# Optimization experiments

Hardware: AMD Instinct MI355X
Metric: run time of the kernel (lower is better)

The kernel has to match this reference:

```python
import jax, jax.numpy as jnp
import numpy as np
from jax import lax

NUM_POINTS = 2048  # M, from init_kwargs


def setup_inputs() -> dict:
    key = jax.random.key(0)
    points = jax.random.normal(key, (16, 65536, 3), dtype=jnp.float32)
    return {"points": points}


def farthest_point_sampling(points, num_samples):
    """Iterative D-FPS. points: (B, N, 3) -> indices (B, M) int32."""
    B, N, _ = points.shape
    BIG = jnp.asarray(1e10, points.dtype)

    def step(carry, _):
        min_dist, last_idx = carry          # (B, N), (B,)
        last_pt = jnp.take_along_axis(points, last_idx[:, None, None], axis=1)  # (B,1,3)
        d = jnp.sum((points - last_pt) ** 2, axis=-1)  # (B, N) squared dist to newest centroid
        min_dist = jnp.minimum(min_dist, d)
        nxt = jnp.argmax(min_dist, axis=1).astype(jnp.int32)  # farthest remaining point
        return (min_dist, nxt), nxt

    first = jnp.zeros((B,), dtype=jnp.int32)  # seed with point 0 (standard FPS convention)
    init = (jnp.full((B, N), BIG, points.dtype), first)
    _, rest = lax.scan(step, init, None, length=num_samples - 1)  # (M-1, B)
    indices = jnp.concatenate([first[None, :], rest], axis=0)      # (M, B)
    return indices.T                                                # (B, M)


def reference(points):
    B, N, _ = points.shape
    if N <= NUM_POINTS:
        idx = jnp.broadcast_to(jnp.arange(N, dtype=jnp.int32)[None, :], (B, N))
        return idx
    return farthest_point_sampling(points, NUM_POINTS)
```

## Files before the change

kernel.cpp:

```cpp
#include <hip/hip_runtime.h>


#define N_PTS   65536
#define M_SAMP  2048
#define NT      512
#define BPB     16
#define PTS_BLK (N_PTS / BPB)
#define PPT     (PTS_BLK / NT)
#define NWAVES  (NT / 64)
#define NBATCH  16
#define SLOT_U64 16
#define NWORK   (BPB * NBATCH)
#define NHEAT   256
#define DONE_MAGIC 0x600D600D600D600Dull

typedef unsigned long long u64;

__device__ __forceinline__ u64 ld_agent(const u64* a) {
  return __hip_atomic_load(a, __ATOMIC_RELAXED, __HIP_MEMORY_SCOPE_AGENT);
}
__device__ __forceinline__ void st_agent(u64* a, u64 v) {
  __hip_atomic_store(a, v, __ATOMIC_RELAXED, __HIP_MEMORY_SCOPE_AGENT);
}
__device__ __forceinline__ u64* done_word(u64* ws, int b) {
  return ws + (size_t)b * BPB * SLOT_U64 + 12;
}

__global__ __launch_bounds__(NT, 2)
void fps_multi(const float* __restrict__ pts, int* __restrict__ out,
               u64* __restrict__ ws) {
  const int t = threadIdx.x;

  if (blockIdx.x >= NWORK) {
    __builtin_amdgcn_s_setprio(0);
    float a0 = 1.0f + t, a1 = 2.0f + t, a2 = 3.0f, a3 = 4.0f;
    float a4 = 5.0f, a5 = 6.0f, a6 = 7.0f, a7 = 8.0f;
    const float k0 = 1.0000001f, k1 = 0.9999991f;
    for (;;) {
      for (int it = 0; it < 128; ++it) {
        a0 = __builtin_fmaf(a0, k0, k1); a1 = __builtin_fmaf(a1, k0, k1);
        a2 = __builtin_fmaf(a2, k0, k1); a3 = __builtin_fmaf(a3, k0, k1);
        a4 = __builtin_fmaf(a4, k0, k1); a5 = __builtin_fmaf(a5, k0, k1);
        a6 = __builtin_fmaf(a6, k0, k1); a7 = __builtin_fmaf(a7, k0, k1);
      }
      const u64 w = ld_agent(done_word(ws, t & 15));
      if (__all(w == DONE_MAGIC)) break;
    }
    const float s = ((a0 + a1) + (a2 + a3)) + ((a4 + a5) + (a6 + a7));
    if (s == -1234.56789f) st_agent(done_word(ws, t & 15) + 1, (u64)t);
    return;
  }

  __builtin_amdgcn_s_setprio(3);
  const int rank = blockIdx.x & (BPB - 1);
  const int b    = blockIdx.x >> 4;
  const float* __restrict__ p = pts + (size_t)b * (size_t)(N_PTS * 3);
  int* __restrict__ o = out + (size_t)b * M_SAMP;
  const int base = rank * PTS_BLK;

  __shared__ float s_pts[PTS_BLK * 3];
  __shared__ u64   s_bv[NWAVES];
  __shared__ int   s_bi[NWAVES];
  __shared__ float s_c[3];

  for (int i = t; i < PTS_BLK * 3; i += NT)
    s_pts[i] = p[base * 3 + i];
  if (rank == 0 && t == 0) o[0] = 0;
  if (t == 0) { s_c[0] = p[0]; s_c[1] = p[1]; s_c[2] = p[2]; }
  __syncthreads();

  double pd[PPT][3];
  double md[PPT];
#pragma unroll
  for (int j = 0; j < PPT; ++j) {
    const int l = t + j * NT;
    pd[j][0] = (double)s_pts[3 * l + 0];
    pd[j][1] = (double)s_pts[3 * l + 1];
    pd[j][2] = (double)s_pts[3 * l + 2];
    md[j] = 1e10;
  }

  for (int m = 1; m < M_SAMP; ++m) {
    const double cx = (double)s_c[0];
    const double cy = (double)s_c[1];
    const double cz = (double)s_c[2];

    u64 bestb = 0;
    int besti = base + t;

#pragma unroll
    for (int j = 0; j < PPT; ++j) {
      const double dx = __dsub_rn(pd[j][0], cx);
      const double dy = __dsub_rn(pd[j][1], cy);
      const double dz = __dsub_rn(pd[j][2], cz);
      const double d  = __dadd_rn(__dadd_rn(__dmul_rn(dx, dx),
                                            __dmul_rn(dy, dy)),
                                  __dmul_rn(dz, dz));
      const double nmd = fmin(md[j], d);
      md[j] = nmd;
      const u64 nb = (u64)__double_as_longlong(nmd);
      if (nb > bestb) { bestb = nb; besti = base + t + j * NT; }
    }

#pragma unroll
    for (int off = 32; off >= 1; off >>= 1) {
      const u64 ov = __shfl_xor(bestb, off, 64);
      const int oi = __shfl_xor(besti, off, 64);
      if (ov > bestb || (ov == bestb && oi < besti)) { bestb = ov; besti = oi; }
    }
    if ((t & 63) == 0) { s_bv[t >> 6] = bestb; s_bi[t >> 6] = besti; }
    __syncthreads();

    if (t < 64) {
      if (t < NWAVES) {
        bestb = s_bv[t]; besti = s_bi[t];
#pragma unroll
        for (int off = NWAVES / 2; off >= 1; off >>= 1) {
          const u64 ov = __shfl_xor(bestb, off, 64);
          const int oi = __shfl_xor(besti, off, 64);
          if (ov > bestb || (ov == bestb && oi < besti)) { bestb = ov; besti = oi; }
        }
      }
      const u64 mm  = (u64)(unsigned)m;
      const u64 grp = (u64)(((m & 1) * NBATCH + b) * BPB);
      if (t == 0) {
        u64* slot = ws + (grp + rank) * SLOT_U64;
        const int l = besti - base;
        const unsigned xb = __float_as_uint(s_pts[3 * l + 0]);
        const unsigned yb = __float_as_uint(s_pts[3 * l + 1]);
        const unsigned zb = __float_as_uint(s_pts[3 * l + 2]);
        const u64 ti = (mm << 16) | (u64)(unsigned)besti;
        st_agent(&slot[0], (bestb << 32) | ti);
        st_agent(&slot[1], (bestb & 0xFFFFFFFF00000000ull) | ti);
        st_agent(&slot[2], ((u64)xb << 32) | (mm << 16) | (u64)(yb >> 16));
        st_agent(&slot[3], ((u64)(yb & 0xFFFFu) << 48) | ((u64)zb << 16) | mm);
      }
      if (t < BPB) {
        const u64* rs = ws + (grp + t) * SLOT_U64;
        u64 A, B, C, D;
        for (;;) {
          A = ld_agent(rs + 0);
          B = ld_agent(rs + 1);
          C = ld_agent(rs + 2);
          D = ld_agent(rs + 3);
          const bool ok = (((A >> 16) & 0xFFFFull) == mm) &
                          (((B >> 16) & 0xFFFFull) == mm) &
                          (((C >> 16) & 0xFFFFull) == mm) &
                          ((D & 0xFFFFull) == mm);
          if (ok) break;
        }
        u64 v = (B & 0xFFFFFFFF00000000ull) | (A >> 32);
        int i = (int)(A & 0xFFFFull);
        float fx = __uint_as_float((unsigned)(C >> 32));
        float fy = __uint_as_float((unsigned)(((C & 0xFFFFull) << 16) | (D >> 48)));
        float fz = __uint_as_float((unsigned)((D >> 16) & 0xFFFFFFFFull));
        int r = t;
#pragma unroll
        for (int off = BPB / 2; off >= 1; off >>= 1) {
          const u64 ov = __shfl_xor(v, off, 64);
          const int oi = __shfl_xor(i, off, 64);
          const int orr = __shfl_xor(r, off, 64);
          if (ov > v || (ov == v && oi < i)) { v = ov; i = oi; r = orr; }
        }
        fx = __shfl(fx, r, 64);
        fy = __shfl(fy, r, 64);
        fz = __shfl(fz, r, 64);
        if (t == 0) {
          s_c[0] = fx; s_c[1] = fy; s_c[2] = fz;
          if (rank == 0) o[m] = i;
        }
      }
    }
    __syncthreads();
  }

  if (rank == 0 && t == 0) st_agent(done_word(ws, b), DONE_MAGIC);
}

extern "C" void kernel_launch(void* const* d_in, const int* in_sizes, int n_in,
                              void* d_out, int out_size, void* d_ws, size_t ws_size,
                              hipStream_t stream) {
  const float* pts = (const float*)d_in[0];
  int* out = (int*)d_out;
  hipLaunchKernelGGL(fps_multi, dim3(NWORK + NHEAT), dim3(NT), 0, stream,
                     pts, out, (u64*)d_ws);
}
```

Baseline: 6.138 ms.

## Remove heater blocks and drop per-iteration second barrier via redundant per-wave exchange

Every wave now redundantly performs the block-level reduction and polls the cross-block workspace slots itself. The centroid is then broadcast within each wave through shuffles instead of shared memory. This removes the second __syncthreads per sample iteration, with per-wave partial results double-buffered by iteration parity to avoid races. It also deletes the extra spinning 'heater' blocks and their done-flag signalling. The trade-off is that many more waves poll global memory concurrently, and any clock or priority effect the heater blocks had is lost.

```diff
diff --git a/kernel.cpp b/kernel.cpp
--- a/kernel.cpp
+++ b/kernel.cpp
@@ -10,9 +10,6 @@
 #define NWAVES  (NT / 64)
 #define NBATCH  16
 #define SLOT_U64 16
-#define NWORK   (BPB * NBATCH)
-#define NHEAT   256
-#define DONE_MAGIC 0x600D600D600D600Dull
 
 typedef unsigned long long u64;
 
@@ -22,51 +19,27 @@
 __device__ __forceinline__ void st_agent(u64* a, u64 v) {
   __hip_atomic_store(a, v, __ATOMIC_RELAXED, __HIP_MEMORY_SCOPE_AGENT);
 }
-__device__ __forceinline__ u64* done_word(u64* ws, int b) {
-  return ws + (size_t)b * BPB * SLOT_U64 + 12;
-}
 
 __global__ __launch_bounds__(NT, 2)
 void fps_multi(const float* __restrict__ pts, int* __restrict__ out,
                u64* __restrict__ ws) {
-  const int t = threadIdx.x;
-
-  if (blockIdx.x >= NWORK) {
-    __builtin_amdgcn_s_setprio(0);
-    float a0 = 1.0f + t, a1 = 2.0f + t, a2 = 3.0f, a3 = 4.0f;
-    float a4 = 5.0f, a5 = 6.0f, a6 = 7.0f, a7 = 8.0f;
-    const float k0 = 1.0000001f, k1 = 0.9999991f;
-    for (;;) {
-      for (int it = 0; it < 128; ++it) {
-        a0 = __builtin_fmaf(a0, k0, k1); a1 = __builtin_fmaf(a1, k0, k1);
-        a2 = __builtin_fmaf(a2, k0, k1); a3 = __builtin_fmaf(a3, k0, k1);
-        a4 = __builtin_fmaf(a4, k0, k1); a5 = __builtin_fmaf(a5, k0, k1);
-        a6 = __builtin_fmaf(a6, k0, k1); a7 = __builtin_fmaf(a7, k0, k1);
-      }
-      const u64 w = ld_agent(done_word(ws, t & 15));
-      if (__all(w == DONE_MAGIC)) break;
-    }
-    const float s = ((a0 + a1) + (a2 + a3)) + ((a4 + a5) + (a6 + a7));
-    if (s == -1234.56789f) st_agent(done_word(ws, t & 15) + 1, (u64)t);
-    return;
-  }
-
-  __builtin_amdgcn_s_setprio(3);
   const int rank = blockIdx.x & (BPB - 1);
   const int b    = blockIdx.x >> 4;
   const float* __restrict__ p = pts + (size_t)b * (size_t)(N_PTS * 3);
   int* __restrict__ o = out + (size_t)b * M_SAMP;
+  const int t    = threadIdx.x;
+  const int lane = t & 63;
+  const int wave = t >> 6;
   const int base = rank * PTS_BLK;
 
   __shared__ float s_pts[PTS_BLK * 3];
-  __shared__ u64   s_bv[NWAVES];
-  __shared__ int   s_bi[NWAVES];
-  __shared__ float s_c[3];
+  __shared__ u64   s_wv[2][NWAVES];
+  __shared__ int   s_wi[2][NWAVES];
 
   for (int i = t; i < PTS_BLK * 3; i += NT)
     s_pts[i] = p[base * 3 + i];
   if (rank == 0 && t == 0) o[0] = 0;
-  if (t == 0) { s_c[0] = p[0]; s_c[1] = p[1]; s_c[2] = p[2]; }
+  float c0 = p[0], c1 = p[1], c2 = p[2];
   __syncthreads();
 
   double pd[PPT][3];
@@ -81,9 +54,9 @@
   }
 
   for (int m = 1; m < M_SAMP; ++m) {
-    const double cx = (double)s_c[0];
-    const double cy = (double)s_c[1];
-    const double cz = (double)s_c[2];
+    const double cx = (double)c0;
+    const double cy = (double)c1;
+    const double cz = (double)c2;
 
     u64 bestb = 0;
     int besti = base + t;
@@ -108,73 +81,76 @@
       const int oi = __shfl_xor(besti, off, 64);
       if (ov > bestb || (ov == bestb && oi < besti)) { bestb = ov; besti = oi; }
     }
-    if ((t & 63) == 0) { s_bv[t >> 6] = bestb; s_bi[t >> 6] = besti; }
+
+    const int par = m & 1;
+    if (lane == 0) { s_wv[par][wave] = bestb; s_wi[par][wave] = besti; }
     __syncthreads();
 
-    if (t < 64) {
-      if (t < NWAVES) {
-        bestb = s_bv[t]; besti = s_bi[t];
+    u64 bb; int bi;
+    if (lane < NWAVES) { bb = s_wv[par][lane]; bi = s_wi[par][lane]; }
+    else               { bb = 0;               bi = 0x7FFFFFFF; }
 #pragma unroll
-        for (int off = NWAVES / 2; off >= 1; off >>= 1) {
-          const u64 ov = __shfl_xor(bestb, off, 64);
-          const int oi = __shfl_xor(besti, off, 64);
-          if (ov > bestb || (ov == bestb && oi < besti)) { bestb = ov; besti = oi; }
-        }
+    for (int off = NWAVES / 2; off >= 1; off >>= 1) {
+      const u64 ov = __shfl_xor(bb, off, 64);
+      const int oi = __shfl_xor(bi, off, 64);
+      if (ov > bb || (ov == bb && oi < bi)) { bb = ov; bi = oi; }
+    }
+
+    const u64 mm  = (u64)(unsigned)m;
+    const u64 grp = (u64)((par * NBATCH + b) * BPB);
+    if (t == 0) {
+      u64* slot = ws + (grp + rank) * SLOT_U64;
+      const int l = bi - base;
+      const unsigned xb = __float_as_uint(s_pts[3 * l + 0]);
+      const unsigned yb = __float_as_uint(s_pts[3 * l + 1]);
+      const unsigned zb = __float_as_uint(s_pts[3 * l + 2]);
+      const u64 ti = (mm << 16) | (u64)(unsigned)bi;
+      st_agent(&slot[0], (bb << 32) | ti);
+      st_agent(&slot[1], (bb & 0xFFFFFFFF00000000ull) | ti);
+      st_agent(&slot[2], ((u64)xb << 32) | (mm << 16) | (u64)(yb >> 16));
+      st_agent(&slot[3], ((u64)(yb & 0xFFFFu) << 48) | ((u64)zb << 16) | mm);
+    }
+
+    float fx = 0.0f, fy = 0.0f, fz = 0.0f;
+    int   wi = 0;
+    if (lane < BPB) {
+      const u64* rs = ws + (grp + lane) * SLOT_U64;
+      u64 A, B, C, D;
+      for (;;) {
+        A = ld_agent(rs + 0);
+        B = ld_agent(rs + 1);
+        C = ld_agent(rs + 2);
+        D = ld_agent(rs + 3);
+        const bool ok = (((A >> 16) & 0xFFFFull) == mm) &
+                        (((B >> 16) & 0xFFFFull) == mm) &
+                        (((C >> 16) & 0xFFFFull) == mm) &
+                        ((D & 0xFFFFull) == mm);
+        if (ok) break;
       }
-      const u64 mm  = (u64)(unsigned)m;
-      const u64 grp = (u64)(((m & 1) * NBATCH + b) * BPB);
-      if (t == 0) {
-        u64* slot = ws + (grp + rank) * SLOT_U64;
-        const int l = besti - base;
-        const unsigned xb = __float_as_uint(s_pts[3 * l + 0]);
-        const unsigned yb = __float_as_uint(s_pts[3 * l + 1]);
-        const unsigned zb = __float_as_uint(s_pts[3 * l + 2]);
-        const u64 ti = (mm << 16) | (u64)(unsigned)besti;
-        st_agent(&slot[0], (bestb << 32) | ti);
-        st_agent(&slot[1], (bestb & 0xFFFFFFFF00000000ull) | ti);
-        st_agent(&slot[2], ((u64)xb << 32) | (mm << 16) | (u64)(yb >> 16));
-        st_agent(&slot[3], ((u64)(yb & 0xFFFFu) << 48) | ((u64)zb << 16) | mm);
+      u64 v = (B & 0xFFFFFFFF00000000ull) | (A >> 32);
+      int i = (int)(A & 0xFFFFull);
+      float gx = __uint_as_float((unsigned)(C >> 32));
+      float gy = __uint_as_float((unsigned)(((C & 0xFFFFull) << 16) | (D >> 48)));
+      float gz = __uint_as_float((unsigned)((D >> 16) & 0xFFFFFFFFull));
+      int r = lane;
+#pragma unroll
+      for (int off = BPB / 2; off >= 1; off >>= 1) {
+        const u64 ov = __shfl_xor(v, off, 64);
+        const int oi = __shfl_xor(i, off, 64);
+        const int orr = __shfl_xor(r, off, 64);
+        if (ov > v || (ov == v && oi < i)) { v = ov; i = oi; r = orr; }
       }
-      if (t < BPB) {
-        const u64* rs = ws + (grp + t) * SLOT_U64;
-        u64 A, B, C, D;
-        for (;;) {
-          A = ld_agent(rs + 0);
-          B = ld_agent(rs + 1);
-          C = ld_agent(rs + 2);
-          D = ld_agent(rs + 3);
-          const bool ok = (((A >> 16) & 0xFFFFull) == mm) &
-                          (((B >> 16) & 0xFFFFull) == mm) &
-                          (((C >> 16) & 0xFFFFull) == mm) &
-                          ((D & 0xFFFFull) == mm);
-          if (ok) break;
-        }
-        u64 v = (B & 0xFFFFFFFF00000000ull) | (A >> 32);
-        int i = (int)(A & 0xFFFFull);
-        float fx = __uint_as_float((unsigned)(C >> 32));
-        float fy = __uint_as_float((unsigned)(((C & 0xFFFFull) << 16) | (D >> 48)));
-        float fz = __uint_as_float((unsigned)((D >> 16) & 0xFFFFFFFFull));
-        int r = t;
-#pragma unroll
-        for (int off = BPB / 2; off >= 1; off >>= 1) {
-          const u64 ov = __shfl_xor(v, off, 64);
-          const int oi = __shfl_xor(i, off, 64);
-          const int orr = __shfl_xor(r, off, 64);
-          if (ov > v || (ov == v && oi < i)) { v = ov; i = oi; r = orr; }
-        }
-        fx = __shfl(fx, r, 64);
-        fy = __shfl(fy, r, 64);
-        fz = __shfl(fz, r, 64);
-        if (t == 0) {
-          s_c[0] = fx; s_c[1] = fy; s_c[2] = fz;
-          if (rank == 0) o[m] = i;
-        }
-      }
+      fx = __shfl(gx, r, 64);
+      fy = __shfl(gy, r, 64);
+      fz = __shfl(gz, r, 64);
+      wi = i;
     }
-    __syncthreads();
+    fx = __shfl(fx, 0, 64);
+    fy = __shfl(fy, 0, 64);
+    fz = __shfl(fz, 0, 64);
+    c0 = fx; c1 = fy; c2 = fz;
+    if (rank == 0 && t == 0) o[m] = wi;
   }
-
-  if (rank == 0 && t == 0) st_agent(done_word(ws, b), DONE_MAGIC);
 }
 
 extern "C" void kernel_launch(void* const* d_in, const int* in_sizes, int n_in,
@@ -182,6 +158,6 @@
                               hipStream_t stream) {
   const float* pts = (const float*)d_in[0];
   int* out = (int*)d_out;
-  hipLaunchKernelGGL(fps_multi, dim3(NWORK + NHEAT), dim3(NT), 0, stream,
+  hipLaunchKernelGGL(fps_multi, dim3(BPB * NBATCH), dim3(NT), 0, stream,
                      pts, out, (u64*)d_ws);
 }
```

Result: slower. 9.296 ms (+51.4%).

## Use 8 blocks of 1024 threads per batch and drop heater blocks

Applied to the files above, without the earlier changes.

Reorganizes the split so that each batch uses 8 cooperating blocks of 1024 threads instead of 16 blocks of 512. This halves the number of blocks taking part in the per-iteration cross-block handshake. It also removes the busy-spinning 'heater' blocks and the priority settings, which were presumably meant to keep clocks high. Each block now handles twice as many points per thread, so the launch uses fewer CUs. It may also lose whatever clock-boosting effect the heater blocks gave.

```diff
diff --git a/kernel.cpp b/kernel.cpp
--- a/kernel.cpp
+++ b/kernel.cpp
@@ -3,16 +3,13 @@
 
 #define N_PTS   65536
 #define M_SAMP  2048
-#define NT      512
-#define BPB     16
+#define NT      1024
+#define BPB     8
 #define PTS_BLK (N_PTS / BPB)
 #define PPT     (PTS_BLK / NT)
 #define NWAVES  (NT / 64)
 #define NBATCH  16
 #define SLOT_U64 16
-#define NWORK   (BPB * NBATCH)
-#define NHEAT   256
-#define DONE_MAGIC 0x600D600D600D600Dull
 
 typedef unsigned long long u64;
 
@@ -22,46 +19,22 @@
 __device__ __forceinline__ void st_agent(u64* a, u64 v) {
   __hip_atomic_store(a, v, __ATOMIC_RELAXED, __HIP_MEMORY_SCOPE_AGENT);
 }
-__device__ __forceinline__ u64* done_word(u64* ws, int b) {
-  return ws + (size_t)b * BPB * SLOT_U64 + 12;
-}
 
-__global__ __launch_bounds__(NT, 2)
+__global__ __launch_bounds__(NT)
 void fps_multi(const float* __restrict__ pts, int* __restrict__ out,
                u64* __restrict__ ws) {
-  const int t = threadIdx.x;
-
-  if (blockIdx.x >= NWORK) {
-    __builtin_amdgcn_s_setprio(0);
-    float a0 = 1.0f + t, a1 = 2.0f + t, a2 = 3.0f, a3 = 4.0f;
-    float a4 = 5.0f, a5 = 6.0f, a6 = 7.0f, a7 = 8.0f;
-    const float k0 = 1.0000001f, k1 = 0.9999991f;
-    for (;;) {
-      for (int it = 0; it < 128; ++it) {
-        a0 = __builtin_fmaf(a0, k0, k1); a1 = __builtin_fmaf(a1, k0, k1);
-        a2 = __builtin_fmaf(a2, k0, k1); a3 = __builtin_fmaf(a3, k0, k1);
-        a4 = __builtin_fmaf(a4, k0, k1); a5 = __builtin_fmaf(a5, k0, k1);
-        a6 = __builtin_fmaf(a6, k0, k1); a7 = __builtin_fmaf(a7, k0, k1);
-      }
-      const u64 w = ld_agent(done_word(ws, t & 15));
-      if (__all(w == DONE_MAGIC)) break;
-    }
-    const float s = ((a0 + a1) + (a2 + a3)) + ((a4 + a5) + (a6 + a7));
-    if (s == -1234.56789f) st_agent(done_word(ws, t & 15) + 1, (u64)t);
-    return;
-  }
-
-  __builtin_amdgcn_s_setprio(3);
   const int rank = blockIdx.x & (BPB - 1);
-  const int b    = blockIdx.x >> 4;
+  const int b    = blockIdx.x >> 3;
   const float* __restrict__ p = pts + (size_t)b * (size_t)(N_PTS * 3);
   int* __restrict__ o = out + (size_t)b * M_SAMP;
+  const int t = threadIdx.x;
   const int base = rank * PTS_BLK;
 
   __shared__ float s_pts[PTS_BLK * 3];
-  __shared__ u64   s_bv[NWAVES];
-  __shared__ int   s_bi[NWAVES];
+  __shared__ u64   s_wv[NWAVES];
+  __shared__ int   s_wi[NWAVES];
   __shared__ float s_c[3];
+  __shared__ int   s_widx;
 
   for (int i = t; i < PTS_BLK * 3; i += NT)
     s_pts[i] = p[base * 3 + i];
@@ -108,21 +81,20 @@
       const int oi = __shfl_xor(besti, off, 64);
       if (ov > bestb || (ov == bestb && oi < besti)) { bestb = ov; besti = oi; }
     }
-    if ((t & 63) == 0) { s_bv[t >> 6] = bestb; s_bi[t >> 6] = besti; }
+    if ((t & 63) == 0) { s_wv[t >> 6] = bestb; s_wi[t >> 6] = besti; }
     __syncthreads();
 
     if (t < 64) {
-      if (t < NWAVES) {
-        bestb = s_bv[t]; besti = s_bi[t];
+      if (t < NWAVES) { bestb = s_wv[t]; besti = s_wi[t]; }
+      else            { bestb = 0;       besti = 0x7FFFFFFF; }
 #pragma unroll
-        for (int off = NWAVES / 2; off >= 1; off >>= 1) {
-          const u64 ov = __shfl_xor(bestb, off, 64);
-          const int oi = __shfl_xor(besti, off, 64);
-          if (ov > bestb || (ov == bestb && oi < besti)) { bestb = ov; besti = oi; }
-        }
+      for (int off = NWAVES / 2; off >= 1; off >>= 1) {
+        const u64 ov = __shfl_xor(bestb, off, 64);
+        const int oi = __shfl_xor(besti, off, 64);
+        if (ov > bestb || (ov == bestb && oi < besti)) { bestb = ov; besti = oi; }
       }
       const u64 mm  = (u64)(unsigned)m;
-      const u64 grp = (u64)(((m & 1) * NBATCH + b) * BPB);
+      const u64 grp = (u64)((((m & 1) * NBATCH + b) * BPB));
       if (t == 0) {
         u64* slot = ws + (grp + rank) * SLOT_U64;
         const int l = besti - base;
@@ -151,9 +123,9 @@
         }
         u64 v = (B & 0xFFFFFFFF00000000ull) | (A >> 32);
         int i = (int)(A & 0xFFFFull);
-        float fx = __uint_as_float((unsigned)(C >> 32));
-        float fy = __uint_as_float((unsigned)(((C & 0xFFFFull) << 16) | (D >> 48)));
-        float fz = __uint_as_float((unsigned)((D >> 16) & 0xFFFFFFFFull));
+        float gx = __uint_as_float((unsigned)(C >> 32));
+        float gy = __uint_as_float((unsigned)(((C & 0xFFFFull) << 16) | (D >> 48)));
+        float gz = __uint_as_float((unsigned)((D >> 16) & 0xFFFFFFFFull));
         int r = t;
 #pragma unroll
         for (int off = BPB / 2; off >= 1; off >>= 1) {
@@ -162,19 +134,19 @@
           const int orr = __shfl_xor(r, off, 64);
           if (ov > v || (ov == v && oi < i)) { v = ov; i = oi; r = orr; }
         }
-        fx = __shfl(fx, r, 64);
-        fy = __shfl(fy, r, 64);
-        fz = __shfl(fz, r, 64);
+        gx = __shfl(gx, r, 64);
+        gy = __shfl(gy, r, 64);
+        gz = __shfl(gz, r, 64);
         if (t == 0) {
-          s_c[0] = fx; s_c[1] = fy; s_c[2] = fz;
+          s_c[0] = gx; s_c[1] = gy; s_c[2] = gz;
+          s_widx = i;
           if (rank == 0) o[m] = i;
         }
       }
     }
     __syncthreads();
+    (void)s_widx;
   }
-
-  if (rank == 0 && t == 0) st_agent(done_word(ws, b), DONE_MAGIC);
 }
 
 extern "C" void kernel_launch(void* const* d_in, const int* in_sizes, int n_in,
@@ -182,6 +154,6 @@
                               hipStream_t stream) {
   const float* pts = (const float*)d_in[0];
   int* out = (int*)d_out;
-  hipLaunchKernelGGL(fps_multi, dim3(NWORK + NHEAT), dim3(NT), 0, stream,
+  hipLaunchKernelGGL(fps_multi, dim3(BPB * NBATCH), dim3(NT), 0, stream,
                      pts, out, (u64*)d_ws);
 }
```

After: 6.529 ms. 6.4% more time.
